# Performance work log

Measured on AMD Instinct MI355X. Metric: run time of the kernel, lower is better.

## Reference

```python
import jax, jax.numpy as jnp
import numpy as np
from jax.scipy.special import logsumexp

B = 64          # batch
SIZE = 256      # lattice width -> SIZE+1 states
LEN_PAT = 32    # pattern length
NEG = -1e9      # finite stand-in for -inf (exp underflows to 0 exactly in fp32)


def setup_inputs() -> dict:
    key = jax.random.key(0)
    k1, k2, k3, k4 = jax.random.split(key, 4)
    logits = jax.random.normal(k1, (B, 3, SIZE), dtype=jnp.float32)
    Q = jax.random.normal(k2, (1, 3, SIZE + 1, SIZE + 1), dtype=jnp.float32) * 0.1
    pattern = jax.random.randint(k3, (LEN_PAT,), 0, 3, dtype=jnp.int32)
    ls = jax.random.randint(k4, (B,), 0, SIZE, dtype=jnp.int32)
    return {"logits": logits, "Q": Q, "pattern": pattern, "ls": ls}


def build_P(logits):
    # Faithful vectorization of P_: P[b,ch,i,j] = sum_{k=i}^{j-1} log y[b,ch,k] if j>i,
    # -inf for j<=i (rows 0..SIZE-1), and row SIZE is all zeros (never masked in the loop).
    C = jax.nn.log_softmax(logits, axis=1)                              # [B,3,SIZE]
    cs = jnp.concatenate([jnp.zeros_like(C[..., :1]), jnp.cumsum(C, -1)], -1)  # [B,3,SIZE+1]
    diff = cs[:, :, None, :] - cs[:, :, :, None]                        # cs[j]-cs[i]
    idx = jnp.arange(SIZE + 1)
    upper = idx[None, :] > idx[:, None]                                 # j > i
    P = jnp.where(upper, diff, NEG)                                     # [B,3,S+1,S+1]
    P = P.at[:, :, SIZE, :].set(0.0)
    return P


def sum_alpha(P, Q, pattern):
    bs, s1 = P.shape[0], P.shape[-1]
    a0 = jnp.full((bs, s1), NEG, dtype=P.dtype).at[:, 0].set(0.0)
    n0 = jnp.zeros((bs,), dtype=P.dtype)  # logsumexp(a0) == 0

    def step(carry, c):
        la, ln = carry
        T = P[:, c] + Q[0, c]                       # [B,S+1,S+1]
        a = logsumexp(T + la[:, :, None], axis=1)   # reduce over source state
        n = ln + logsumexp(a, axis=-1)
        a = a + (ln - n)[:, None]                   # online renormalization
        return (a, n), a + n[:, None]

    _, outs = jax.lax.scan(step, (a0, n0), pattern)            # [LEN,B,S+1]
    return jnp.concatenate([a0[:, None, :], jnp.transpose(outs, (1, 0, 2))], axis=1)


def sum_beta(P, Q, pattern, ls):
    bs, s1 = P.shape[0], P.shape[-1]
    b0 = jnp.full((bs, s1), NEG, dtype=P.dtype).at[jnp.arange(bs), ls].set(0.0)
    n0 = jnp.zeros((bs,), dtype=P.dtype)

    def step(carry, c):
        lb, ln = carry
        T = P[:, c] + Q[0, c]
        b = logsumexp(T + lb[:, None, :], axis=2)   # reduce over target state
        n = ln + logsumexp(b, axis=-1)
        b = b + (ln - n)[:, None]
        return (b, n), b + n[:, None]

    _, outs = jax.lax.scan(step, (b0, n0), pattern[::-1])      # positions LEN-1..0
    outs = jnp.flip(jnp.transpose(outs, (1, 0, 2)), axis=1)    # positions 0..LEN-1
    return jnp.concatenate([outs, b0[:, None, :]], axis=1)


def reference(logits, Q, pattern, ls):
    bs = logits.shape[0]
    P = build_P(logits)                                         # [B,3,S+1,S+1]
    a = sum_alpha(P, Q, pattern)                                # [B,LEN+1,S+1]
    b = sum_beta(P, Q, pattern, ls)                             # [B,LEN+1,S+1]
    ll = a + b
    M = a[jnp.arange(bs), -1, ls]                               # [B]
    p = a + b - M[:, None, None]                                # single marginals
    Tpat = P[:, pattern] + Q[0][pattern]                        # [B,LEN,S+1,S+1]
    t = a[:, :-1, :, None] + b[:, 1:, None, :] + Tpat - M[:, None, None, None]
    return (M, ll, a, b, ls, p, t)
```

## Files before the change

kernel.cpp:

```cpp
#include <hip/hip_runtime.h>

#define NEGV (-1e9f)

typedef float vf4 __attribute__((ext_vector_type(4)));

constexpr int BN   = 64;
constexpr int S1   = 257;
constexpr int LEN  = 32;
constexpr int CH   = S1 * S1;
constexpr int ROWS = LEN + 1;
constexpr int ABSZ = BN * ROWS * S1;
constexpr int EQP  = 260;
constexpr int EQC  = S1 * EQP;

constexpr int OFF_M  = 0;
constexpr int OFF_LL = 64;
constexpr int OFF_A  = OFF_LL + ABSZ;
constexpr int OFF_B  = OFF_A + ABSZ;
constexpr int OFF_LS = OFF_B + ABSZ;
constexpr int OFF_P  = OFF_LS + 64;
constexpr int OFF_T  = OFF_P + ABSZ;

constexpr int WS_CS  = 0;
constexpr int WS_M   = 64 * 771;
constexpr int WS_SCR = WS_M + 64;

constexpr int SC_CSD = 0;
constexpr int SC_EQ  = 2 * 64 * 771;
constexpr int SC_EQT = SC_EQ + 3 * EQC;
constexpr int SC_END = SC_EQT + 3 * EQC;

__device__ __forceinline__ double dexp(double x) {
  double t = x * 1.4426950408889634;
  double n = floor(t);
  float  f = (float)(t - n);
  double r = (double)exp2f(f);
  long long bb = __double_as_longlong(r);
  bb += ((long long)n) << 52;
  return __longlong_as_double(bb);
}
__device__ __forceinline__ float dlogf(double x) {
  if (!(x > 1e-300)) return NEGV;
  long long bb = __double_as_longlong(x);
  int e = (int)((bb >> 52) & 0x7ff) - 1023;
  bb = (bb & 0xFFFFFFFFFFFFFLL) | 0x3FF0000000000000LL;
  float m = (float)__longlong_as_double(bb);
  return __logf(m) + (float)e * 0.69314718055994531f;
}

__device__ __forceinline__ void barL() {
  asm volatile("s_waitcnt lgkmcnt(0)" ::: "memory");
  __builtin_amdgcn_s_barrier();
  __builtin_amdgcn_sched_barrier(0);
}

__global__ __launch_bounds__(256) void k_pre(const float* __restrict__ logits,
                                             const float* __restrict__ Q,
                                             const int* __restrict__ ls,
                                             float* __restrict__ ws,
                                             float* __restrict__ scr,
                                             float* __restrict__ out) {
  const int blk = blockIdx.x;
  const int tid = threadIdx.x;
  if (blk < 3 * S1) {
    const int c = blk / S1, i = blk - c * S1;
    float* EQ = scr + SC_EQ;
    const float* Qr = Q + c * CH + i * S1;
    for (int j = tid; j < S1; j += 256) {
      float e = __expf(Qr[j]);
      EQ[c * EQC + i * EQP + j] = ((i < j) || (i == 256)) ? e : 0.f;
    }
    return;
  }
  if (blk < 3 * S1 + 51) {
    const int g = blk - 3 * S1;
    const int c = g / 17, grp = g - c * 17;
    const int i = grp * 16 + (tid & 15);
    float* EQT = scr + SC_EQT;
    if (i < S1) {
      const float* Qci = Q + c * CH + i * S1;
      for (int j = tid >> 4; j < S1; j += 16) {
        float e = __expf(Qci[j]);
        EQT[c * EQC + j * EQP + i] = ((j > i) || (j == 256)) ? e : 0.f;
      }
    }
    return;
  }
  const int b = blk - 3 * S1 - 51;
  __shared__ float sC[3][256];
  {
    float l0 = logits[(b*3+0)*256 + tid];
    float l1 = logits[(b*3+1)*256 + tid];
    float l2 = logits[(b*3+2)*256 + tid];
    float mm = fmaxf(l0, fmaxf(l1, l2));
    float lse = mm + __logf(__expf(l0-mm) + __expf(l1-mm) + __expf(l2-mm));
    sC[0][tid] = l0 - lse;
    sC[1][tid] = l1 - lse;
    sC[2][tid] = l2 - lse;
  }
  __syncthreads();
  const int w = tid >> 6, lane = tid & 63;
  double* csD = (double*)(scr + SC_CSD);
  if (w < 3) {
    float*  cs32 = ws + WS_CS + b*771 + w*257;
    double* csd  = csD + b*771 + w*257;
    if (lane == 0) { cs32[0] = 0.f; csd[0] = 0.0; }
    double carry = 0.0;
    for (int t = 0; t < 4; ++t) {
      double v = (double)sC[w][t*64 + lane];
      #pragma unroll
      for (int off = 1; off < 64; off <<= 1) {
        double o = __shfl_up(v, off);
        if (lane >= off) v += o;
      }
      double r = carry + v;
      cs32[t*64 + lane + 1] = (float)r;
      csd [t*64 + lane + 1] = r;
      carry += __shfl(v, 63);
    }
  }
  if (tid == 0) out[OFF_LS + b] = (float)ls[b];
}

__global__ __launch_bounds__(512, 2) void k_rec(const float* __restrict__ scr,
                                                const int* __restrict__ pattern,
                                                const int* __restrict__ ls,
                                                float* __restrict__ ws,
                                                float* __restrict__ out) {
  __shared__ double ecsP[3][257], ecsM[3][257];
  __shared__ double wDp[2][258];
  __shared__ double AD[258];
  __shared__ double part[8][260];
  __shared__ float eqR[3][257];
  __shared__ float eqC[3][257];
  __shared__ int patS[LEN];
  const int tid = threadIdx.x;
  const bool isBeta = (blockIdx.x >= BN);
  const int b = isBeta ? (blockIdx.x - BN) : blockIdx.x;
  const float* EQ  = scr + SC_EQ;
  const float* EQT = scr + SC_EQT;
  const double* csD = (const double*)(scr + SC_CSD) + b * 771;

  if (tid < LEN) patS[tid] = pattern[tid];
  const int lsb = ls[b];
  for (int idx = tid; idx < 771; idx += 512) {
    int c = idx / 257, j = idx - c * 257;
    double x = csD[idx];
    ecsP[c][j] = dexp(x);
    ecsM[c][j] = dexp(-x);
    eqR[c][j] = EQ[c * EQC + 256 * EQP + j];
    eqC[c][j] = EQ[c * EQC + j * EQP + 256];
  }
  float* outab = out + (isBeta ? OFF_B : OFF_A) + b * (ROWS * S1);
  const int w = tid >> 6, l = tid & 63;
  const int k0 = w << 5, col0 = l << 2;
  const bool act = isBeta ? (col0 < k0 + 31) : (k0 < col0 + 3);

  if (tid < S1) {
    if (!isBeta) {
      __builtin_nontemporal_store((tid == 0) ? 0.f : NEGV, &outab[tid]);
    } else {
      AD[tid] = (tid == lsb) ? 1.0 : 0.0;
      __builtin_nontemporal_store((tid == lsb) ? 0.f : NEGV, &outab[LEN * S1 + tid]);
    }
  }
  __syncthreads();
  if (tid < S1) {
    if (!isBeta) wDp[0][tid] = (tid == 0) ? 1.0 : 0.0;
    else         wDp[0][tid] = (tid == lsb) ? ecsP[patS[LEN-1]][tid] : 0.0;
  }
  float4 tile[32];
  {
    const float* bp = (isBeta ? EQT : EQ) +
                      (isBeta ? patS[LEN-1] : patS[0]) * EQC + k0 * EQP + col0;
    if (act) {
      #pragma unroll
      for (int kk = 0; kk < 32; ++kk) tile[kk] = *(const float4*)(bp + kk * EQP);
    }
  }
  barL();

  int cur = 0;
  if (!isBeta) {
    for (int step = 0; step < LEN; ++step, cur ^= 1) {
      const int c = patS[step];
      const double* wc = wDp[cur];
      double a0 = 0, a1 = 0, a2 = 0, a3 = 0;
      if (act) {
        #pragma unroll
        for (int kk = 0; kk < 32; ++kk) {
          float4 e = tile[kk];
          double wv = wc[k0 + kk];
          a0 += wv * (double)e.x;
          a1 += wv * (double)e.y;
          a2 += wv * (double)e.z;
          a3 += wv * (double)e.w;
        }
        if (step + 1 < LEN) {
          const float* bp = EQ + patS[step+1] * EQC + k0 * EQP + col0;
          #pragma unroll
          for (int kk = 0; kk < 32; ++kk) tile[kk] = *(const float4*)(bp + kk * EQP);
        }
      }
      part[w][col0] = a0; part[w][col0+1] = a1;
      part[w][col0+2] = a2; part[w][col0+3] = a3;
      double c2 = 0;
      if (l < 32) c2 = wc[k0 + l] * (double)eqC[c][k0 + l];
      c2 += __shfl_xor(c2, 1); c2 += __shfl_xor(c2, 2);
      c2 += __shfl_xor(c2, 4); c2 += __shfl_xor(c2, 8); c2 += __shfl_xor(c2, 16);
      if (l == 0) part[w][256] = c2;
      barL();
      if (tid < S1) {
        const int j = tid;
        const double wA256 = wDp[cur][256];
        double sum = ((part[0][j] + part[1][j]) + (part[2][j] + part[3][j]))
                   + ((part[4][j] + part[5][j]) + (part[6][j] + part[7][j]));
        double Ar = ecsP[c][j] * sum + wA256 * (double)eqR[c][j];
        float lo = dlogf(Ar);
        __builtin_nontemporal_store(lo, &outab[(step + 1) * S1 + j]);
        if (step == LEN - 1) {
          if (j == lsb) { out[OFF_M + b] = lo; ws[WS_M + b] = lo; }
        } else {
          wDp[cur ^ 1][j] = (j < 256) ? Ar * ecsM[patS[step+1]][j] : Ar;
        }
      }
      barL();
    }
  } else {
    for (int ss = 0; ss < LEN; ++ss, cur ^= 1) {
      const int step = LEN - 1 - ss;
      const int c = patS[step];
      const double* wc = wDp[cur];
      double a0 = 0, a1 = 0, a2 = 0, a3 = 0;
      if (act) {
        #pragma unroll
        for (int kk = 0; kk < 32; ++kk) {
          float4 e = tile[kk];
          double wv = wc[k0 + kk];
          a0 += wv * (double)e.x;
          a1 += wv * (double)e.y;
          a2 += wv * (double)e.z;
          a3 += wv * (double)e.w;
        }
        if (ss + 1 < LEN) {
          const float* bp = EQT + patS[step-1] * EQC + k0 * EQP + col0;
          #pragma unroll
          for (int kk = 0; kk < 32; ++kk) tile[kk] = *(const float4*)(bp + kk * EQP);
        }
      }
      part[w][col0] = a0; part[w][col0+1] = a1;
      part[w][col0+2] = a2; part[w][col0+3] = a3;
      double r2 = 0;
      if (l < 32) r2 = AD[k0 + l] * (double)eqR[c][k0 + l];
      r2 += __shfl_xor(r2, 1); r2 += __shfl_xor(r2, 2);
      r2 += __shfl_xor(r2, 4); r2 += __shfl_xor(r2, 8); r2 += __shfl_xor(r2, 16);
      if (l == 0) part[w][256] = r2;
      barL();
      if (tid < S1) {
        const int i = tid;
        const double wB256 = wDp[cur][256];
        double sum = ((part[0][i] + part[1][i]) + (part[2][i] + part[3][i]))
                   + ((part[4][i] + part[5][i]) + (part[6][i] + part[7][i]));
        double Ar;
        if (i < 256) Ar = ecsM[c][i] * (sum + (double)eqC[c][i] * wB256);
        else         Ar = sum + (double)eqR[c][256] * AD[256];
        __builtin_nontemporal_store(dlogf(Ar), &outab[step * S1 + i]);
        AD[i] = Ar;
        if (ss < LEN - 1) wDp[cur ^ 1][i] = Ar * ecsP[patS[step-1]][i];
      }
      barL();
    }
  }
}

__global__ __launch_bounds__(256) void k_llp(const float* __restrict__ ws,
                                             float* __restrict__ out) {
  int idx = blockIdx.x * 256 + threadIdx.x;
  if (idx >= ABSZ) return;
  int b = idx / (ROWS * S1);
  float a = out[OFF_A + idx];
  float bb = out[OFF_B + idx];
  float ll = a + bb;
  __builtin_nontemporal_store(ll, out + OFF_LL + idx);
  __builtin_nontemporal_store(ll - ws[WS_M + b], out + OFF_P + idx);
}

__global__ __launch_bounds__(256) void k_t(const float* __restrict__ Q,
                                           const int* __restrict__ pattern,
                                           const float* __restrict__ ws,
                                           float* __restrict__ out) {
  __shared__ float qs[32 * 257];
  __shared__ float c1[257], c2[257], r1[32], r2[32];
  __shared__ int Kc[3][32];
  __shared__ int nK[3];
  const int tid  = threadIdx.x;
  const int slab = blockIdx.x >> 6;
  const int slot = blockIdx.x & 63;
  if (tid == 0) {
    int n0 = 0, n1 = 0, n2 = 0;
    for (int k = 0; k < LEN; ++k) {
      int c = pattern[k];
      if (c == 0) Kc[0][n0++] = k;
      else if (c == 1) Kc[1][n1++] = k;
      else Kc[2][n2++] = k;
    }
    nK[0] = n0; nK[1] = n1; nK[2] = n2;
  }
  __syncthreads();
  int c, chunk;
  {
    const int s0 = 2 * nK[0], s1 = s0 + 2 * nK[1];
    if (slot < s0)      { c = 0; chunk = slot; }
    else if (slot < s1) { c = 1; chunk = slot - s0; }
    else                { c = 2; chunk = slot - s1; }
  }
  const int nk = nK[c];
  const int i0 = slab << 5;
  const int R  = (257 - i0 < 32) ? (257 - i0) : 32;
  for (int idx = tid; idx < R * 257; idx += 256)
    qs[idx] = Q[c * CH + i0 * 257 + idx];
  const int p0 = chunk << 5;
  for (int pp = 0; pp < 32; ++pp) {
    const int p = p0 + pp;
    const int b = p / nk, kidx = p - b * nk;
    const int k = Kc[c][kidx];
    __syncthreads();
    const float Mb = ws[WS_M + b];
    const float* cs = ws + WS_CS + b * 771 + c * 257;
    const float* ar = out + OFF_A + (b * ROWS + k) * S1;
    const float* br = out + OFF_B + (b * ROWS + k + 1) * S1;
    for (int j = tid; j < S1; j += 256) {
      float bv = br[j], cv = cs[j];
      c1[j] = bv + cv;
      c2[j] = bv;
    }
    if (tid < R) {
      const int i = i0 + tid;
      float av = ar[i];
      r1[tid] = av - cs[i] - Mb;
      r2[tid] = av - Mb + ((i == 256) ? 0.f : NEGV);
    }
    __syncthreads();
    const int bk2 = (b << 5) + k;
    float* tb = out + OFF_T + (size_t)bk2 * CH + i0 * 257;
    const int N = R * 257;
    const int lead = (4 - ((bk2 + i0) & 3)) & 3;
    const int main4 = (N - lead) >> 2;
    const int tail = N - lead - (main4 << 2);
    if (tid < lead) {
      const int sp = tid;
      float v = (sp > i0) ? (r1[0] + c1[sp]) : (r2[0] + c2[sp]);
      __builtin_nontemporal_store(qs[sp] + v, tb + sp);
    }
    if (tid >= 8 && tid < 8 + tail) {
      const int sp = lead + (main4 << 2) + (tid - 8);
      const int ii = sp / 257, j = sp - ii * 257;
      float v = (j > i0 + ii) ? (r1[ii] + c1[j]) : (r2[ii] + c2[j]);
      __builtin_nontemporal_store(qs[sp] + v, tb + sp);
    }
    for (int v4 = tid; v4 < main4; v4 += 256) {
      const int base = lead + (v4 << 2);
      int ii = base / 257, j = base - ii * 257;
      const float* qp = qs + base;
      vf4 o;
      o.x = qp[0] + ((j > i0 + ii) ? (r1[ii] + c1[j]) : (r2[ii] + c2[j]));
      ++j; if (j == 257) { j = 0; ++ii; }
      o.y = qp[1] + ((j > i0 + ii) ? (r1[ii] + c1[j]) : (r2[ii] + c2[j]));
      ++j; if (j == 257) { j = 0; ++ii; }
      o.z = qp[2] + ((j > i0 + ii) ? (r1[ii] + c1[j]) : (r2[ii] + c2[j]));
      ++j; if (j == 257) { j = 0; ++ii; }
      o.w = qp[3] + ((j > i0 + ii) ? (r1[ii] + c1[j]) : (r2[ii] + c2[j]));
      __builtin_nontemporal_store(o, (vf4*)(tb + base));
    }
  }
}

extern "C" void kernel_launch(void* const* d_in, const int* in_sizes, int n_in,
                              void* d_out, int out_size, void* d_ws, size_t ws_size,
                              hipStream_t stream) {
  const float* logits = (const float*)d_in[0];
  const float* Q      = (const float*)d_in[1];
  const int* pattern  = (const int*)d_in[2];
  const int* ls       = (const int*)d_in[3];
  float* out = (float*)d_out;
  float* ws  = (float*)d_ws;

  const size_t need = (size_t)(WS_SCR + SC_END) * sizeof(float);
  float* scr = (ws_size >= need) ? (ws + WS_SCR) : (out + OFF_T);

  k_pre<<<3*S1 + 51 + BN, 256, 0, stream>>>(logits, Q, ls, ws, scr, out);
  k_rec<<<2*BN, 512, 0, stream>>>(scr, pattern, ls, ws, out);
  k_llp<<<(ABSZ + 255)/256, 256, 0, stream>>>(ws, out);
  k_t<<<9 * 64, 256, 0, stream>>>(Q, pattern, ws, out);
}
```

Measured before the change: 278.6 us.

## Merge alpha and beta recursions into one 1024-thread block per batch

```diff
diff --git a/kernel.cpp b/kernel.cpp
--- a/kernel.cpp
+++ b/kernel.cpp
@@ -122,154 +122,133 @@
   if (tid == 0) out[OFF_LS + b] = (float)ls[b];
 }
 
-__global__ __launch_bounds__(512, 2) void k_rec(const float* __restrict__ scr,
-                                                const int* __restrict__ pattern,
-                                                const int* __restrict__ ls,
-                                                float* __restrict__ ws,
-                                                float* __restrict__ out) {
-  __shared__ double ecsP[3][257], ecsM[3][257];
-  __shared__ double wDp[2][258];
+__global__ __launch_bounds__(1024) void k_rec(const float* __restrict__ scr,
+                                              const int* __restrict__ pattern,
+                                              const int* __restrict__ ls,
+                                              float* __restrict__ ws,
+                                              float* __restrict__ out) {
+  __shared__ double csDs[771];
+  __shared__ double wA[2][258];
+  __shared__ double wB[2][258];
   __shared__ double AD[258];
-  __shared__ double part[8][260];
+  __shared__ double partA[8][260];
+  __shared__ double partB[8][260];
   __shared__ float eqR[3][257];
   __shared__ float eqC[3][257];
   __shared__ int patS[LEN];
   const int tid = threadIdx.x;
-  const bool isBeta = (blockIdx.x >= BN);
-  const int b = isBeta ? (blockIdx.x - BN) : blockIdx.x;
+  const int b = blockIdx.x;
   const float* EQ  = scr + SC_EQ;
   const float* EQT = scr + SC_EQT;
   const double* csD = (const double*)(scr + SC_CSD) + b * 771;
 
   if (tid < LEN) patS[tid] = pattern[tid];
   const int lsb = ls[b];
-  for (int idx = tid; idx < 771; idx += 512) {
+  for (int idx = tid; idx < 771; idx += 1024) {
     int c = idx / 257, j = idx - c * 257;
-    double x = csD[idx];
-    ecsP[c][j] = dexp(x);
-    ecsM[c][j] = dexp(-x);
+    csDs[idx] = csD[idx];
     eqR[c][j] = EQ[c * EQC + 256 * EQP + j];
     eqC[c][j] = EQ[c * EQC + j * EQP + 256];
   }
-  float* outab = out + (isBeta ? OFF_B : OFF_A) + b * (ROWS * S1);
+  float* outA = out + OFF_A + b * (ROWS * S1);
+  float* outB = out + OFF_B + b * (ROWS * S1);
   const int w = tid >> 6, l = tid & 63;
-  const int k0 = w << 5, col0 = l << 2;
+  const bool isBeta = (w >= 8);
+  const int wl = w & 7;
+  const int k0 = wl << 5, col0 = l << 2;
   const bool act = isBeta ? (col0 < k0 + 31) : (k0 < col0 + 3);
 
-  if (tid < S1) {
-    if (!isBeta) {
-      __builtin_nontemporal_store((tid == 0) ? 0.f : NEGV, &outab[tid]);
-    } else {
-      AD[tid] = (tid == lsb) ? 1.0 : 0.0;
-      __builtin_nontemporal_store((tid == lsb) ? 0.f : NEGV, &outab[LEN * S1 + tid]);
-    }
-  }
   __syncthreads();
   if (tid < S1) {
-    if (!isBeta) wDp[0][tid] = (tid == 0) ? 1.0 : 0.0;
-    else         wDp[0][tid] = (tid == lsb) ? ecsP[patS[LEN-1]][tid] : 0.0;
-  }
-  float4 tile[32];
-  {
-    const float* bp = (isBeta ? EQT : EQ) +
-                      (isBeta ? patS[LEN-1] : patS[0]) * EQC + k0 * EQP + col0;
-    if (act) {
-      #pragma unroll
-      for (int kk = 0; kk < 32; ++kk) tile[kk] = *(const float4*)(bp + kk * EQP);
-    }
+    wA[0][tid] = (tid == 0) ? 1.0 : 0.0;
+    __builtin_nontemporal_store((tid == 0) ? 0.f : NEGV, &outA[tid]);
+    AD[tid] = (tid == lsb) ? 1.0 : 0.0;
+    wB[0][tid] = (tid == lsb) ? dexp(csDs[patS[LEN-1]*257 + tid]) : 0.0;
+    __builtin_nontemporal_store((tid == lsb) ? 0.f : NEGV, &outB[LEN * S1 + tid]);
   }
   barL();
 
   int cur = 0;
-  if (!isBeta) {
-    for (int step = 0; step < LEN; ++step, cur ^= 1) {
-      const int c = patS[step];
-      const double* wc = wDp[cur];
+  for (int s = 0; s < LEN; ++s, cur ^= 1) {
+    if (!isBeta) {
+      const int c = patS[s];
+      const double* wc = wA[cur];
       double a0 = 0, a1 = 0, a2 = 0, a3 = 0;
       if (act) {
-        #pragma unroll
+        const float* bp = EQ + c * EQC + k0 * EQP + col0;
+        #pragma unroll 8
         for (int kk = 0; kk < 32; ++kk) {
-          float4 e = tile[kk];
+          float4 e = *(const float4*)(bp + kk * EQP);
           double wv = wc[k0 + kk];
           a0 += wv * (double)e.x;
           a1 += wv * (double)e.y;
           a2 += wv * (double)e.z;
           a3 += wv * (double)e.w;
         }
-        if (step + 1 < LEN) {
-          const float* bp = EQ + patS[step+1] * EQC + k0 * EQP + col0;
-          #pragma unroll
-          for (int kk = 0; kk < 32; ++kk) tile[kk] = *(const float4*)(bp + kk * EQP);
-        }
-      }
-      part[w][col0] = a0; part[w][col0+1] = a1;
-      part[w][col0+2] = a2; part[w][col0+3] = a3;
+      }
+      partA[wl][col0] = a0; partA[wl][col0+1] = a1;
+      partA[wl][col0+2] = a2; partA[wl][col0+3] = a3;
       double c2 = 0;
       if (l < 32) c2 = wc[k0 + l] * (double)eqC[c][k0 + l];
       c2 += __shfl_xor(c2, 1); c2 += __shfl_xor(c2, 2);
       c2 += __shfl_xor(c2, 4); c2 += __shfl_xor(c2, 8); c2 += __shfl_xor(c2, 16);
-      if (l == 0) part[w][256] = c2;
-      barL();
-      if (tid < S1) {
-        const int j = tid;
-        const double wA256 = wDp[cur][256];
-        double sum = ((part[0][j] + part[1][j]) + (part[2][j] + part[3][j]))
-                   + ((part[4][j] + part[5][j]) + (part[6][j] + part[7][j]));
-        double Ar = ecsP[c][j] * sum + wA256 * (double)eqR[c][j];
-        float lo = dlogf(Ar);
-        __builtin_nontemporal_store(lo, &outab[(step + 1) * S1 + j]);
-        if (step == LEN - 1) {
-          if (j == lsb) { out[OFF_M + b] = lo; ws[WS_M + b] = lo; }
-        } else {
-          wDp[cur ^ 1][j] = (j < 256) ? Ar * ecsM[patS[step+1]][j] : Ar;
-        }
-      }
-      barL();
-    }
-  } else {
-    for (int ss = 0; ss < LEN; ++ss, cur ^= 1) {
-      const int step = LEN - 1 - ss;
-      const int c = patS[step];
-      const double* wc = wDp[cur];
+      if (l == 0) partA[wl][256] = c2;
+    } else {
+      const int stepb = LEN - 1 - s;
+      const int c = patS[stepb];
+      const double* wc = wB[cur];
       double a0 = 0, a1 = 0, a2 = 0, a3 = 0;
       if (act) {
-        #pragma unroll
+        const float* bp = EQT + c * EQC + k0 * EQP + col0;
+        #pragma unroll 8
         for (int kk = 0; kk < 32; ++kk) {
-          float4 e = tile[kk];
+          float4 e = *(const float4*)(bp + kk * EQP);
           double wv = wc[k0 + kk];
           a0 += wv * (double)e.x;
           a1 += wv * (double)e.y;
           a2 += wv * (double)e.z;
           a3 += wv * (double)e.w;
         }
-        if (ss + 1 < LEN) {
-          const float* bp = EQT + patS[step-1] * EQC + k0 * EQP + col0;
-          #pragma unroll
-          for (int kk = 0; kk < 32; ++kk) tile[kk] = *(const float4*)(bp + kk * EQP);
-        }
-      }
-      part[w][col0] = a0; part[w][col0+1] = a1;
-      part[w][col0+2] = a2; part[w][col0+3] = a3;
+      }
+      partB[wl][col0] = a0; partB[wl][col0+1] = a1;
+      partB[wl][col0+2] = a2; partB[wl][col0+3] = a3;
       double r2 = 0;
       if (l < 32) r2 = AD[k0 + l] * (double)eqR[c][k0 + l];
       r2 += __shfl_xor(r2, 1); r2 += __shfl_xor(r2, 2);
       r2 += __shfl_xor(r2, 4); r2 += __shfl_xor(r2, 8); r2 += __shfl_xor(r2, 16);
-      if (l == 0) part[w][256] = r2;
-      barL();
-      if (tid < S1) {
-        const int i = tid;
-        const double wB256 = wDp[cur][256];
-        double sum = ((part[0][i] + part[1][i]) + (part[2][i] + part[3][i]))
-                   + ((part[4][i] + part[5][i]) + (part[6][i] + part[7][i]));
-        double Ar;
-        if (i < 256) Ar = ecsM[c][i] * (sum + (double)eqC[c][i] * wB256);
-        else         Ar = sum + (double)eqR[c][256] * AD[256];
-        __builtin_nontemporal_store(dlogf(Ar), &outab[step * S1 + i]);
-        AD[i] = Ar;
-        if (ss < LEN - 1) wDp[cur ^ 1][i] = Ar * ecsP[patS[step-1]][i];
-      }
-      barL();
-    }
+      if (l == 0) partB[wl][256] = r2;
+    }
+    barL();
+    if (tid < S1) {
+      const int c = patS[s];
+      const int j = tid;
+      const double wA256 = wA[cur][256];
+      double sum = ((partA[0][j] + partA[1][j]) + (partA[2][j] + partA[3][j]))
+                 + ((partA[4][j] + partA[5][j]) + (partA[6][j] + partA[7][j]));
+      double Ar = dexp(csDs[c*257 + j]) * sum + wA256 * (double)eqR[c][j];
+      float lo = dlogf(Ar);
+      __builtin_nontemporal_store(lo, &outA[(s + 1) * S1 + j]);
+      if (s == LEN - 1) {
+        if (j == lsb) { out[OFF_M + b] = lo; ws[WS_M + b] = lo; }
+      } else {
+        const int cn = patS[s + 1];
+        wA[cur ^ 1][j] = (j < 256) ? Ar * dexp(-csDs[cn*257 + j]) : Ar;
+      }
+    } else if (tid >= 512 && tid < 512 + S1) {
+      const int stepb = LEN - 1 - s;
+      const int c = patS[stepb];
+      const int i = tid - 512;
+      const double wB256 = wB[cur][256];
+      double sum = ((partB[0][i] + partB[1][i]) + (partB[2][i] + partB[3][i]))
+                 + ((partB[4][i] + partB[5][i]) + (partB[6][i] + partB[7][i]));
+      double Br;
+      if (i < 256) Br = dexp(-csDs[c*257 + i]) * (sum + (double)eqC[c][i] * wB256);
+      else         Br = sum + (double)eqR[c][256] * AD[256];
+      __builtin_nontemporal_store(dlogf(Br), &outB[stepb * S1 + i]);
+      AD[i] = Br;
+      if (s < LEN - 1) wB[cur ^ 1][i] = Br * dexp(csDs[patS[stepb-1]*257 + i]);
+    }
+    barL();
   }
 }
 
@@ -389,7 +368,7 @@
   float* scr = (ws_size >= need) ? (ws + WS_SCR) : (out + OFF_T);
 
   k_pre<<<3*S1 + 51 + BN, 256, 0, stream>>>(logits, Q, ls, ws, scr, out);
-  k_rec<<<2*BN, 512, 0, stream>>>(scr, pattern, ls, ws, out);
+  k_rec<<<BN, 1024, 0, stream>>>(scr, pattern, ls, ws, out);
   k_llp<<<(ABSZ + 255)/256, 256, 0, stream>>>(ws, out);
   k_t<<<9 * 64, 256, 0, stream>>>(Q, pattern, ws, out);
 }
```

Measured after the change: 309.3 us. 11.0% more time.
